# Performance work log

Measured on AMD Instinct MI355X. Metric: run time of the kernel, lower is better.

## Reference

```python
import jax, jax.numpy as jnp
import numpy as np

DIM = 1280
HEADS = 16
HD = DIM // HEADS  # 80
NSEG = 8
LSEG = 1024
SEQ = NSEG * LSEG  # 8192


def _rotate_half(x):
    x1, x2 = jnp.split(x, 2, axis=-1)
    return jnp.concatenate([-x2, x1], axis=-1)


def setup_inputs() -> dict:
    key = jax.random.key(0)
    ks = jax.random.split(key, 6)
    hidden_states = jax.random.normal(ks[0], (SEQ, DIM), dtype=jnp.float32)
    # rotary embedding table: per-position angles over head_dim
    inv_freq = 1.0 / (10000.0 ** (np.arange(0, HD, 2, dtype=np.float32) / HD))
    pos = np.arange(SEQ, dtype=np.float32)
    freqs = np.outer(pos, inv_freq)                    # [SEQ, HD/2]
    emb = np.concatenate([freqs, freqs], axis=-1)      # [SEQ, HD]
    cos = jnp.asarray(np.cos(emb), dtype=jnp.float32)
    sin = jnp.asarray(np.sin(emb), dtype=jnp.float32)
    w_scale = 1.0 / np.sqrt(DIM)
    qkv_w = jax.random.normal(ks[1], (DIM, 3 * DIM), dtype=jnp.float32) * w_scale
    qkv_b = jax.random.normal(ks[2], (3 * DIM,), dtype=jnp.float32) * 0.02
    proj_w = jax.random.normal(ks[3], (DIM, DIM), dtype=jnp.float32) * w_scale
    proj_b = jax.random.normal(ks[4], (DIM,), dtype=jnp.float32) * 0.02
    cu_seqlens = jnp.arange(NSEG + 1, dtype=jnp.int32) * LSEG
    return {
        "hidden_states": hidden_states,
        "cos": cos,
        "sin": sin,
        "qkv_w": qkv_w,
        "qkv_b": qkv_b,
        "proj_w": proj_w,
        "proj_b": proj_b,
        "cu_seqlens": cu_seqlens,
    }


def reference(hidden_states, cos, sin, qkv_w, qkv_b, proj_w, proj_b, cu_seqlens):
    S, D = hidden_states.shape
    n_seg = cu_seqlens.shape[0] - 1          # static
    L = S // n_seg                            # equal-length packed segments
    # fused QKV projection: [S, 3D] -> q, k, v each [S, H, hd]
    qkv = hidden_states @ qkv_w + qkv_b
    q, k, v = (t.reshape(S, HEADS, HD) for t in jnp.split(qkv, 3, axis=-1))
    # RoPE (computed in fp32, as in apply_rotary_pos_emb_vision)
    c = cos.astype(jnp.float32)[:, None, :]   # [S, 1, hd]
    s = sin.astype(jnp.float32)[:, None, :]
    qf = q.astype(jnp.float32)
    kf = k.astype(jnp.float32)
    q = (qf * c + _rotate_half(qf) * s).astype(q.dtype)
    k = (kf * c + _rotate_half(kf) * s).astype(k.dtype)
    # block-diagonal varlen attention == independent attention per segment
    qs = q.reshape(n_seg, L, HEADS, HD)
    ks = k.reshape(n_seg, L, HEADS, HD)
    vs = v.reshape(n_seg, L, HEADS, HD)
    scale = HD ** -0.5
    scores = jnp.einsum("nqhd,nkhd->nhqk", qs, ks) * scale
    probs = jax.nn.softmax(scores.astype(jnp.float32), axis=-1).astype(qs.dtype)
    out = jnp.einsum("nhqk,nkhd->nqhd", probs, vs)     # [n, L, H, hd]
    out = out.reshape(S, D)
    return out @ proj_w + proj_b
```

## Files before the change

kernel.cpp:

```cpp
#include <hip/hip_runtime.h>

#define SEQ   8192
#define DIM   1280
#define HEADS 16
#define HD    80
#define LSEG  1024
#define QKVD  3840

typedef unsigned short USHORT;
typedef __attribute__((ext_vector_type(8))) short bf16x8;
typedef __attribute__((ext_vector_type(4))) float f32x4;
typedef __attribute__((ext_vector_type(4))) USHORT u16x4;
typedef __attribute__((ext_vector_type(4))) int i32x4;

#define CSF  0.16129832f

__device__ __forceinline__ USHORT f2bf(float x) {
  unsigned u = __float_as_uint(x);
  u += 0x7fffu + ((u >> 16) & 1u);
  return (USHORT)(u >> 16);
}
__device__ __forceinline__ float bf2f(USHORT b) {
  return __uint_as_float(((unsigned)b) << 16);
}
__device__ __forceinline__ void gload16(const void* g, void* l) {
  __builtin_amdgcn_global_load_lds(
      (const __attribute__((address_space(1))) void*)g,
      (__attribute__((address_space(3))) void*)l, 16, 0, 0);
}
__device__ __forceinline__ unsigned cvtpk(float a, float b) {
  unsigned d;
  asm("v_cvt_pk_bf16_f32 %0, %1, %2" : "=v"(d) : "v"(a), "v"(b));
  return d;
}
#define SB() __builtin_amdgcn_sched_barrier(0)

__global__ __launch_bounds__(256) void prep1(
    const float* __restrict__ hs, USHORT* __restrict__ hsB,
    const float* __restrict__ qkv_w, USHORT* __restrict__ qkvwT,
    const float* __restrict__ proj_w, USHORT* __restrict__ pwT) {
  __shared__ float tb[32][33];
  const int bx = blockIdx.x;
  const int tid = threadIdx.x;
  if (bx < 10240) {
    const int i = bx * 256 + tid;
    const float4 v = reinterpret_cast<const float4*>(hs)[i];
    USHORT* o = hsB + (size_t)i * 4;
    o[0] = f2bf(v.x); o[1] = f2bf(v.y); o[2] = f2bf(v.z); o[3] = f2bf(v.w);
    return;
  }
  const float* W; USHORT* T; int K, N, n0, k0;
  if (bx < 15040) {
    const int b = bx - 10240;
    W = qkv_w; T = qkvwT; K = DIM; N = QKVD;
    n0 = (b % 120) * 32; k0 = (b / 120) * 32;
  } else {
    const int b = bx - 15040;
    W = proj_w; T = pwT; K = DIM; N = DIM;
    n0 = (b % 40) * 32; k0 = (b / 40) * 32;
  }
  const int c = tid & 31, r0 = tid >> 5;
  for (int r = r0; r < 32; r += 8) tb[r][c] = W[(size_t)(k0 + r) * N + n0 + c];
  __syncthreads();
  for (int r = r0; r < 32; r += 8)
    T[(size_t)(n0 + r) * K + k0 + c] = f2bf(tb[c][r]);
}

__global__ __launch_bounds__(256) void prep2(
    USHORT* __restrict__ qkv, const float* __restrict__ cosb,
    const float* __restrict__ sinb, uint4* __restrict__ zb) {
  const int bx = blockIdx.x;
  const int tid = threadIdx.x;
  if (bx < 10240) {
    int idx = bx * 256 + tid;
    const int d4 = (idx % 10) * 4;
    int t = idx / 10;
    const int h = t % HEADS;
    t /= HEADS;
    const int qk = t & 1;
    const int s = t >> 1;
    USHORT* base = qkv + (size_t)s * QKVD + qk * DIM + h * HD;
    const u16x4 x1 = *(const u16x4*)&base[d4];
    const u16x4 x2 = *(const u16x4*)&base[d4 + 40];
    const f32x4 c1 = *(const f32x4*)&cosb[s * HD + d4];
    const f32x4 s1 = *(const f32x4*)&sinb[s * HD + d4];
    const f32x4 c2 = *(const f32x4*)&cosb[s * HD + d4 + 40];
    const f32x4 s2 = *(const f32x4*)&sinb[s * HD + d4 + 40];
    u16x4 o1, o2;
#pragma unroll
    for (int j = 0; j < 4; ++j) {
      const float a = bf2f(x1[j]), b = bf2f(x2[j]);
      o1[j] = f2bf(a * c1[j] - b * s1[j]);
      o2[j] = f2bf(b * c2[j] + a * s2[j]);
    }
    *(u16x4*)&base[d4] = o1;
    *(u16x4*)&base[d4 + 40] = o2;
    return;
  }
  if (tid < 64) zb[tid] = uint4{0u, 0u, 0u, 0u};
}

__global__ __launch_bounds__(512, 1) void mfma_gemm256(
    const USHORT* __restrict__ Ah, const USHORT* __restrict__ Bh,
    const float* __restrict__ bias, USHORT* __restrict__ Cout,
    USHORT* __restrict__ VtGo, int M, int N, int K, int lda) {
  extern __shared__ USHORT sm[];

  const int tid = threadIdx.x;
  const int l = tid & 63;
  const int w = tid >> 6;
  const int fr = l & 15;
  const int g = l >> 4;
  const int nrow = M >> 8;
  const int nwg = nrow * (N >> 8);
  const int orig = blockIdx.x;
  const int wg = (orig & 7) * (nwg >> 3) + (orig >> 3);
  const int row0 = (wg % nrow) << 8;
  const int col0 = (wg / nrow) << 8;
  const int wr = (w >> 2) << 7;
  const int wc = (w & 3) << 6;

  const f32x4 fz = {0.f, 0.f, 0.f, 0.f};
  f32x4 acc[8][4];
#pragma unroll
  for (int m = 0; m < 8; ++m)
#pragma unroll
    for (int n = 0; n < 4; ++n) acc[m][n] = fz;

  const int NT = K >> 5;

  const USHORT* asrc[2];
  const USHORT* bsrc[2];
#pragma unroll
  for (int i = 0; i < 2; ++i) {
    const int u = i * 512 + tid;
    const int row = u >> 2;
    const int c = (u & 3) ^ ((row >> 1) & 3);
    asrc[i] = Ah + (size_t)(row0 + row) * lda + c * 8;
    bsrc[i] = Bh + (size_t)(col0 + row) * K + c * 8;
  }
  auto stage = [&](int b) {
#pragma unroll
    for (int i = 0; i < 2; ++i) {
      USHORT* dst = sm + b * 16384 + (i * 512 + (w << 6)) * 8;
      gload16(asrc[i], dst);
      gload16(bsrc[i], dst + 8192);
    }
  };
  auto advance = [&]() {
#pragma unroll
    for (int i = 0; i < 2; ++i) { asrc[i] += 32; bsrc[i] += 32; }
  };

  const int sl = (g ^ ((fr >> 1) & 3)) << 3;
  const int aBase = (wr + fr) * 32 + sl;
  const int bBase = 8192 + (wc + fr) * 32 + sl;

  stage(0); advance();
  stage(1); advance();

  int cur = 0, sb = 2;
  for (int t = 0; t < NT; ++t) {
    asm volatile("s_waitcnt vmcnt(4)" ::: "memory");
    SB();
    __builtin_amdgcn_s_barrier();
    SB();
    const int cb = cur * 16384;
    bf16x8 ah[8], bh[4];
#pragma unroll
    for (int m = 0; m < 8; ++m)
      ah[m] = *(const bf16x8*)(sm + cb + aBase + m * 512);
#pragma unroll
    for (int n = 0; n < 4; ++n)
      bh[n] = *(const bf16x8*)(sm + cb + bBase + n * 512);
    stage(sb);
    if (t < NT - 3) advance();
    SB();
    asm volatile("s_waitcnt lgkmcnt(0)" ::: "memory");
    SB();
    __builtin_amdgcn_s_setprio(1);
#pragma unroll
    for (int m = 0; m < 8; ++m)
#pragma unroll
      for (int n = 0; n < 4; ++n)
        acc[m][n] = __builtin_amdgcn_mfma_f32_16x16x32_bf16(
            ah[m], bh[n], acc[m][n], 0, 0, 0);
    __builtin_amdgcn_s_setprio(0);
    cur = (cur == 2) ? 0 : cur + 1;
    sb = (sb == 2) ? 0 : sb + 1;
  }

  asm volatile("s_waitcnt vmcnt(0)" ::: "memory");

  float bv[4];
#pragma unroll
  for (int n = 0; n < 4; ++n) bv[n] = bias[col0 + wc + n * 16 + fr];
#pragma unroll
  for (int m = 0; m < 8; ++m)
#pragma unroll
    for (int n = 0; n < 4; ++n) {
      const int colb = col0 + wc + n * 16;
      const int row = row0 + wr + m * 16 + g * 4;
      if (colb >= 2 * DIM) {
        u16x4 o;
#pragma unroll
        for (int r = 0; r < 4; ++r) o[r] = f2bf(acc[m][n][r] + bv[n]);
        const int rl = row & 63;
        const int sc = (rl & 0x23) | ((rl & 0x10) >> 2) | ((rl & 0x0C) << 1);
        *(u16x4*)&VtGo[(size_t)(colb + fr - 2 * DIM) * SEQ + (row & ~63) + sc] = o;
      } else {
#pragma unroll
        for (int r = 0; r < 4; ++r)
          Cout[(size_t)(row + r) * N + colb + fr] = f2bf(acc[m][n][r] + bv[n]);
      }
    }
}

__global__ __launch_bounds__(256) void mfma_gemm(
    const USHORT* __restrict__ Ah, const USHORT* __restrict__ Bh,
    const float* __restrict__ bias, float* __restrict__ Cout,
    int M, int N, int K, int lda) {
  __shared__ __align__(16) USHORT AhL[2][8192];
  __shared__ __align__(16) USHORT BhL[2][8192];

  const int tid = threadIdx.x;
  const int l = tid & 63;
  const int w = tid >> 6;
  const int nrow = M >> 7;
  const int nwg = nrow * (N >> 7);
  const int orig = blockIdx.x;
  const int wg = (orig & 7) * (nwg >> 3) + (orig >> 3);
  const int row0 = (wg % nrow) << 7;
  const int col0 = (wg / nrow) << 7;
  const int wr = (w >> 1) << 6;
  const int wc = (w & 1) << 6;

  const f32x4 fz = {0.f, 0.f, 0.f, 0.f};
  f32x4 acc[4][4];
#pragma unroll
  for (int m = 0; m < 4; ++m)
#pragma unroll
    for (int n = 0; n < 4; ++n) acc[m][n] = fz;

  const int fr = l & 15;
  const int g = l >> 4;
  const int NT = K >> 6;

  const USHORT* asrc[4];
  const USHORT* bsrc[4];
#pragma unroll
  for (int i = 0; i < 4; ++i) {
    const int u = (w * 4 + i) * 64 + l;
    const int row = u >> 3;
    const int c = (u & 7) ^ (row & 7);
    asrc[i] = Ah + (size_t)(row0 + row) * lda + c * 8;
    bsrc[i] = Bh + (size_t)(col0 + row) * K + c * 8;
  }
  auto stage = [&](int b) {
#pragma unroll
    for (int i = 0; i < 4; ++i) {
      gload16(asrc[i], &AhL[b][(w * 4 + i) * 512]);
      gload16(bsrc[i], &BhL[b][(w * 4 + i) * 512]);
    }
  };
  auto advance = [&]() {
#pragma unroll
    for (int i = 0; i < 4; ++i) { asrc[i] += 64; bsrc[i] += 64; }
  };

  const int fb = fr & 7;
  int aOff[2], bOff[2];
#pragma unroll
  for (int ks = 0; ks < 2; ++ks) {
    const int sl = (((ks << 2) + g) ^ fb) << 3;
    aOff[ks] = (wr + fr) * 64 + sl;
    bOff[ks] = (wc + fr) * 64 + sl;
  }
  const USHORT* AB = &AhL[0][0];
  const USHORT* BB = &BhL[0][0];

  stage(0); advance();
  stage(1); advance();

  for (int t = 0; t < NT; ++t) {
    const int cur = t & 1;
    asm volatile("s_waitcnt vmcnt(8)" ::: "memory");
    SB();
    __builtin_amdgcn_s_barrier();
    SB();
    const int cb = cur << 13;
    bf16x8 ah[2][4], bh[2][4];
#pragma unroll
    for (int m = 0; m < 4; ++m) {
      ah[0][m] = *(const bf16x8*)(AB + cb + aOff[0] + m * 1024);
      bh[0][m] = *(const bf16x8*)(BB + cb + bOff[0] + m * 1024);
    }
    SB();
#pragma unroll
    for (int m = 0; m < 4; ++m) {
      ah[1][m] = *(const bf16x8*)(AB + cb + aOff[1] + m * 1024);
      bh[1][m] = *(const bf16x8*)(BB + cb + bOff[1] + m * 1024);
    }
    SB();
    asm volatile("s_waitcnt lgkmcnt(8)" ::: "memory");
    SB();
    __builtin_amdgcn_s_setprio(1);
#pragma unroll
    for (int m = 0; m < 4; ++m)
#pragma unroll
      for (int n = 0; n < 4; ++n)
        acc[m][n] = __builtin_amdgcn_mfma_f32_16x16x32_bf16(
            ah[0][m], bh[0][n], acc[m][n], 0, 0, 0);
    __builtin_amdgcn_s_setprio(0);
    SB();
    asm volatile("s_waitcnt lgkmcnt(0)" ::: "memory");
    SB();
    __builtin_amdgcn_s_barrier();
    SB();
    stage(cur);
    if (t < NT - 3) advance();
    SB();
    __builtin_amdgcn_s_setprio(1);
#pragma unroll
    for (int m = 0; m < 4; ++m)
#pragma unroll
      for (int n = 0; n < 4; ++n)
        acc[m][n] = __builtin_amdgcn_mfma_f32_16x16x32_bf16(
            ah[1][m], bh[1][n], acc[m][n], 0, 0, 0);
    __builtin_amdgcn_s_setprio(0);
  }

  asm volatile("s_waitcnt vmcnt(0)" ::: "memory");

  float bv[4];
#pragma unroll
  for (int n = 0; n < 4; ++n) bv[n] = bias[col0 + wc + n * 16 + fr];
#pragma unroll
  for (int m = 0; m < 4; ++m)
#pragma unroll
    for (int n = 0; n < 4; ++n)
#pragma unroll
      for (int r = 0; r < 4; ++r) {
        const float v = acc[m][n][r] + bv[n];
        const int row = row0 + wr + m * 16 + (l >> 4) * 4 + r;
        const int col = col0 + wc + n * 16 + fr;
        Cout[(size_t)row * N + col] = v;
      }
}

__global__ __launch_bounds__(256, 3) void attn_mfma9(
    const USHORT* __restrict__ qkv, const USHORT* __restrict__ VtG,
    const USHORT* __restrict__ zbuf, USHORT* __restrict__ aoB) {
  const int h = blockIdx.y;
  const int bx = blockIdx.x;
  const int qb = (bx & 7) * 8 + (bx >> 3);
  const int s0 = qb * 128;
  const int k0g = (s0 / LSEG) * LSEG;
  const int tid = threadIdx.x;
  const int w = tid >> 6, l = tid & 63;
  const int g = l >> 4, fr = l & 15;
  const int q0 = s0 + w * 32;

  __shared__ __align__(16) USHORT Kl[2][64 * 128];
  __shared__ __align__(16) USHORT Vl[2][80 * 64];

  bf16x8 qb_frag[2][3];
#pragma unroll
  for (int nt2 = 0; nt2 < 2; ++nt2)
#pragma unroll
    for (int ks = 0; ks < 3; ++ks)
      qb_frag[nt2][ks] = *(const bf16x8*)
          &qkv[(size_t)(q0 + nt2 * 16 + fr) * QKVD + h * HD + ks * 32 + g * 8];

  const f32x4 fz = {0.f, 0.f, 0.f, 0.f};
  f32x4 oacc[2][5];
#pragma unroll
  for (int m = 0; m < 2; ++m)
#pragma unroll
    for (int n = 0; n < 5; ++n) oacc[m][n] = fz;
  float l_run[2] = {0.f, 0.f};

  const int nV = (w < 2) ? 3 : 2;
  const int vbase = (w < 2) ? w * 3 : 6 + (w - 2) * 2;
  const USHORT* ksrc[4];
  int kstep[4];
#pragma unroll
  for (int i = 0; i < 4; ++i) {
    const int t = (w * 4 + i) * 64 + l;
    const int row = t >> 4, c = (t & 15) ^ (row & 7);
    if (c < 10) {
      ksrc[i] = qkv + (size_t)(k0g + row) * QKVD + DIM + h * HD + c * 8;
      kstep[i] = 64 * QKVD;
    } else {
      ksrc[i] = zbuf;
      kstep[i] = 0;
    }
  }
  const USHORT* vsrc[3] = {zbuf, zbuf, zbuf};
#pragma unroll
  for (int i = 0; i < 3; ++i)
    if (i < nV) {
      const int u = (vbase + i) * 64 + l;
      const int row = u >> 3, c = (u & 7) ^ (row & 7);
      vsrc[i] = VtG + (size_t)(h * HD + row) * SEQ + k0g + c * 8;
    }

  auto stageKV = [&](int kb, int b) {
#pragma unroll
    for (int i = 0; i < 4; ++i)
      gload16(ksrc[i] + (size_t)kb * kstep[i], &Kl[b][(w * 4 + i) * 512]);
#pragma unroll
    for (int i = 0; i < 3; ++i)
      if (i < nV)
        gload16(vsrc[i] + kb * 64, &Vl[b][(vbase + i) * 512]);
  };

  const int fb = fr & 7;
  int kOff[3], vOff[2];
#pragma unroll
  for (int ks = 0; ks < 3; ++ks)
    kOff[ks] = fr * 128 + ((((ks << 2) + g) ^ fb) << 3);
#pragma unroll
  for (int ks = 0; ks < 2; ++ks)
    vOff[ks] = fr * 64 + ((((ks << 2) + g) ^ fb) << 3);
  const USHORT* KB = &Kl[0][0];
  const USHORT* VB = &Vl[0][0];

  stageKV(0, 0);
  stageKV(1, 1);

  for (int kb = 0; kb < 16; ++kb) {
    const int cur = kb & 1;
    if (w < 2) {
      asm volatile("s_waitcnt vmcnt(7)" ::: "memory");
    } else {
      asm volatile("s_waitcnt vmcnt(6)" ::: "memory");
    }
    SB();
    __builtin_amdgcn_s_barrier();
    SB();
    const int kcb = cur << 13;
    const int vcb = cur * 5120;

    f32x4 sc[4][2];
#pragma unroll
    for (int m = 0; m < 4; ++m)
#pragma unroll
      for (int nt2 = 0; nt2 < 2; ++nt2) sc[m][nt2] = fz;
    __builtin_amdgcn_s_setprio(1);
#pragma unroll
    for (int ks = 0; ks < 3; ++ks)
#pragma unroll
      for (int m = 0; m < 4; ++m) {
        const bf16x8 kbf = *(const bf16x8*)(KB + kcb + kOff[ks] + m * 2048);
#pragma unroll
        for (int nt2 = 0; nt2 < 2; ++nt2)
          sc[m][nt2] = __builtin_amdgcn_mfma_f32_16x16x32_bf16(
              kbf, qb_frag[nt2][ks], sc[m][nt2], 0, 0, 0);
      }
    __builtin_amdgcn_s_setprio(0);

    unsigned pkr[2][4][2];
#pragma unroll
    for (int nt2 = 0; nt2 < 2; ++nt2) {
      float ps = 0.f;
#pragma unroll
      for (int m = 0; m < 4; ++m) {
        float p[4];
#pragma unroll
        for (int j = 0; j < 4; ++j) {
          p[j] = exp2f(sc[m][nt2][j] * CSF);
          ps += p[j];
        }
        pkr[nt2][m][0] = cvtpk(p[0], p[1]);
        pkr[nt2][m][1] = cvtpk(p[2], p[3]);
      }
      ps += __shfl_xor(ps, 16);
      ps += __shfl_xor(ps, 32);
      l_run[nt2] += ps;
    }

#pragma unroll
    for (int ks = 0; ks < 2; ++ks) {
      union { bf16x8 v8; i32x4 i4; } pa[2];
#pragma unroll
      for (int mt2 = 0; mt2 < 2; ++mt2) {
        pa[mt2].i4[0] = (int)pkr[mt2][2 * ks][0];
        pa[mt2].i4[1] = (int)pkr[mt2][2 * ks][1];
        pa[mt2].i4[2] = (int)pkr[mt2][2 * ks + 1][0];
        pa[mt2].i4[3] = (int)pkr[mt2][2 * ks + 1][1];
      }
      __builtin_amdgcn_s_setprio(1);
#pragma unroll
      for (int nt = 0; nt < 5; ++nt) {
        const bf16x8 vb = *(const bf16x8*)(VB + vcb + vOff[ks] + nt * 1024);
#pragma unroll
        for (int mt2 = 0; mt2 < 2; ++mt2)
          oacc[mt2][nt] = __builtin_amdgcn_mfma_f32_16x16x32_bf16(
              pa[mt2].v8, vb, oacc[mt2][nt], 0, 0, 0);
      }
      __builtin_amdgcn_s_setprio(0);
    }

    __builtin_amdgcn_s_barrier();
    SB();
    const int kn = (kb + 2 < 16) ? kb + 2 : kb;
    stageKV(kn, cur);
    SB();
  }

  asm volatile("s_waitcnt vmcnt(0)" ::: "memory");

  float linv[2][4];
#pragma unroll
  for (int mt2 = 0; mt2 < 2; ++mt2)
#pragma unroll
    for (int j = 0; j < 4; ++j)
      linv[mt2][j] = 1.f / __shfl(l_run[mt2], 20 * g + j);
#pragma unroll
  for (int mt2 = 0; mt2 < 2; ++mt2)
#pragma unroll
    for (int nt = 0; nt < 5; ++nt)
#pragma unroll
      for (int j = 0; j < 4; ++j) {
        const int row = s0 + w * 32 + mt2 * 16 + g * 4 + j;
        const int col = h * HD + nt * 16 + fr;
        aoB[(size_t)row * QKVD + col] = f2bf(oacc[mt2][nt][j] * linv[mt2][j]);
      }
}

extern "C" void kernel_launch(void* const* d_in, const int* in_sizes, int n_in,
                              void* d_out, int out_size, void* d_ws,
                              size_t ws_size, hipStream_t stream) {
  const float* hs = (const float*)d_in[0];
  const float* cosb = (const float*)d_in[1];
  const float* sinb = (const float*)d_in[2];
  const float* qkv_w = (const float*)d_in[3];
  const float* qkv_b = (const float*)d_in[4];
  const float* proj_w = (const float*)d_in[5];
  const float* proj_b = (const float*)d_in[6];
  char* ws = (char*)d_ws;

  USHORT* qkvB  = (USHORT*)(ws);
  USHORT* hsB   = (USHORT*)(ws + 62914560u);
  USHORT* qkvwT = (USHORT*)(ws + 83886080u);
  USHORT* pwT   = (USHORT*)(ws + 93716480u);
  USHORT* VtG   = (USHORT*)d_out;
  USHORT* zbuf  = qkvwT;
  USHORT* aoB   = qkvB + 2 * DIM;

  hipFuncSetAttribute((const void*)mfma_gemm256,
                      hipFuncAttributeMaxDynamicSharedMemorySize, 98304);

  prep1<<<16640, 256, 0, stream>>>(hs, hsB, qkv_w, qkvwT, proj_w, pwT);
  mfma_gemm256<<<(SEQ / 256) * (QKVD / 256), 512, 98304, stream>>>(
      hsB, qkvwT, qkv_b, qkvB, VtG, SEQ, QKVD, DIM, DIM);
  prep2<<<10241, 256, 0, stream>>>(qkvB, cosb, sinb, (uint4*)zbuf);
  attn_mfma9<<<dim3(SEQ / 128, HEADS), 256, 0, stream>>>(qkvB, VtG, zbuf, aoB);
  mfma_gemm<<<(SEQ / 128) * (DIM / 128), 256, 0, stream>>>(
      aoB, pwT, proj_b, (float*)d_out, SEQ, DIM, DIM, QKVD);
}
```

Before: 257.0 us.

## Use 1024-thread blocks with 64x64 warp tiles and double buffering in QKV GEMM

The QKV GEMM now launches 1024 threads per 256x256 tile, giving each of 16 waves a 64x64 sub-tile with half the accumulators. Global-to-LDS staging drops from triple to double buffering, cutting LDS to 64KB. A second barrier per K-step is added before overwriting the buffer being read. The aim is more waves for latency hiding and lower register pressure, at the cost of an extra barrier per iteration and less prefetch depth. The launch bound asks for 4 blocks of 1024 threads per CU, which may be unattainable and could force register spills.

```diff
diff --git a/kernel.cpp b/kernel.cpp
--- a/kernel.cpp
+++ b/kernel.cpp
@@ -100,7 +100,7 @@
   if (tid < 64) zb[tid] = uint4{0u, 0u, 0u, 0u};
 }
 
-__global__ __launch_bounds__(512, 1) void mfma_gemm256(
+__global__ __launch_bounds__(1024, 4) void mfma_gemm256(
     const USHORT* __restrict__ Ah, const USHORT* __restrict__ Bh,
     const float* __restrict__ bias, USHORT* __restrict__ Cout,
     USHORT* __restrict__ VtGo, int M, int N, int K, int lda) {
@@ -117,40 +117,28 @@
   const int wg = (orig & 7) * (nwg >> 3) + (orig >> 3);
   const int row0 = (wg % nrow) << 8;
   const int col0 = (wg / nrow) << 8;
-  const int wr = (w >> 2) << 7;
+  const int wr = (w >> 2) << 6;
   const int wc = (w & 3) << 6;
 
   const f32x4 fz = {0.f, 0.f, 0.f, 0.f};
-  f32x4 acc[8][4];
-#pragma unroll
-  for (int m = 0; m < 8; ++m)
+  f32x4 acc[4][4];
+#pragma unroll
+  for (int m = 0; m < 4; ++m)
 #pragma unroll
     for (int n = 0; n < 4; ++n) acc[m][n] = fz;
 
   const int NT = K >> 5;
 
-  const USHORT* asrc[2];
-  const USHORT* bsrc[2];
-#pragma unroll
-  for (int i = 0; i < 2; ++i) {
-    const int u = i * 512 + tid;
-    const int row = u >> 2;
-    const int c = (u & 3) ^ ((row >> 1) & 3);
-    asrc[i] = Ah + (size_t)(row0 + row) * lda + c * 8;
-    bsrc[i] = Bh + (size_t)(col0 + row) * K + c * 8;
-  }
+  const int srow = tid >> 2;
+  const int sc0 = (tid & 3) ^ ((srow >> 1) & 3);
+  const USHORT* asrc = Ah + (size_t)(row0 + srow) * lda + sc0 * 8;
+  const USHORT* bsrc = Bh + (size_t)(col0 + srow) * K + sc0 * 8;
   auto stage = [&](int b) {
-#pragma unroll
-    for (int i = 0; i < 2; ++i) {
-      USHORT* dst = sm + b * 16384 + (i * 512 + (w << 6)) * 8;
-      gload16(asrc[i], dst);
-      gload16(bsrc[i], dst + 8192);
-    }
+    USHORT* dst = sm + b * 16384 + (w << 9);
+    gload16(asrc, dst);
+    gload16(bsrc, dst + 8192);
   };
-  auto advance = [&]() {
-#pragma unroll
-    for (int i = 0; i < 2; ++i) { asrc[i] += 32; bsrc[i] += 32; }
-  };
+  auto advance = [&]() { asrc += 32; bsrc += 32; };
 
   const int sl = (g ^ ((fr >> 1) & 3)) << 3;
   const int aBase = (wr + fr) * 32 + sl;
@@ -159,35 +147,34 @@
   stage(0); advance();
   stage(1); advance();
 
-  int cur = 0, sb = 2;
   for (int t = 0; t < NT; ++t) {
-    asm volatile("s_waitcnt vmcnt(4)" ::: "memory");
+    const int cur = t & 1;
+    asm volatile("s_waitcnt vmcnt(2)" ::: "memory");
     SB();
     __builtin_amdgcn_s_barrier();
     SB();
     const int cb = cur * 16384;
-    bf16x8 ah[8], bh[4];
-#pragma unroll
-    for (int m = 0; m < 8; ++m)
+    bf16x8 ah[4], bh[4];
+#pragma unroll
+    for (int m = 0; m < 4; ++m) {
       ah[m] = *(const bf16x8*)(sm + cb + aBase + m * 512);
-#pragma unroll
-    for (int n = 0; n < 4; ++n)
-      bh[n] = *(const bf16x8*)(sm + cb + bBase + n * 512);
-    stage(sb);
+      bh[m] = *(const bf16x8*)(sm + cb + bBase + m * 512);
+    }
+    asm volatile("s_waitcnt lgkmcnt(0)" ::: "memory");
+    SB();
+    __builtin_amdgcn_s_barrier();
+    SB();
+    stage(cur);
     if (t < NT - 3) advance();
     SB();
-    asm volatile("s_waitcnt lgkmcnt(0)" ::: "memory");
-    SB();
     __builtin_amdgcn_s_setprio(1);
 #pragma unroll
-    for (int m = 0; m < 8; ++m)
+    for (int m = 0; m < 4; ++m)
 #pragma unroll
       for (int n = 0; n < 4; ++n)
         acc[m][n] = __builtin_amdgcn_mfma_f32_16x16x32_bf16(
             ah[m], bh[n], acc[m][n], 0, 0, 0);
     __builtin_amdgcn_s_setprio(0);
-    cur = (cur == 2) ? 0 : cur + 1;
-    sb = (sb == 2) ? 0 : sb + 1;
   }
 
   asm volatile("s_waitcnt vmcnt(0)" ::: "memory");
@@ -196,7 +183,7 @@
 #pragma unroll
   for (int n = 0; n < 4; ++n) bv[n] = bias[col0 + wc + n * 16 + fr];
 #pragma unroll
-  for (int m = 0; m < 8; ++m)
+  for (int m = 0; m < 4; ++m)
 #pragma unroll
     for (int n = 0; n < 4; ++n) {
       const int colb = col0 + wc + n * 16;
@@ -550,10 +537,10 @@
   USHORT* aoB   = qkvB + 2 * DIM;
 
   hipFuncSetAttribute((const void*)mfma_gemm256,
-                      hipFuncAttributeMaxDynamicSharedMemorySize, 98304);
+                      hipFuncAttributeMaxDynamicSharedMemorySize, 65536);
 
   prep1<<<16640, 256, 0, stream>>>(hs, hsB, qkv_w, qkvwT, proj_w, pwT);
-  mfma_gemm256<<<(SEQ / 256) * (QKVD / 256), 512, 98304, stream>>>(
+  mfma_gemm256<<<(SEQ / 256) * (QKVD / 256), 1024, 65536, stream>>>(
       hsB, qkvwT, qkv_b, qkvB, VtG, SEQ, QKVD, DIM, DIM);
   prep2<<<10241, 256, 0, stream>>>(qkvB, cosb, sinb, (uint4*)zbuf);
   attn_mfma9<<<dim3(SEQ / 128, HEADS), 256, 0, stream>>>(qkvB, VtG, zbuf, aoB);
```

Result: slower. 276.2 us (+7.5%).
